# Kernel optimization log

Hardware: AMD Instinct MI355X
Metric: run time of the kernel (lower is better)

The kernel has to match this reference:

```python
import jax, jax.numpy as jnp
import numpy as np

N = 100000
H = 4      # heads
C = 32     # hidden per head (out_channels)
DIN = 9
NEG_SLOPE = 0.2  # PyG GATConv default


def gat_layer(x, src, dst, W, a_src, a_dst, b):
    # x: [N, F] -> h: [N, H, C]
    h = (x @ W).reshape(-1, H, C)
    s = (h * a_src).sum(-1)  # [N, H]
    d = (h * a_dst).sum(-1)  # [N, H]
    alpha = jax.nn.leaky_relu(s[src] + d[dst], negative_slope=NEG_SLOPE)  # [E, H]
    # segment softmax over incoming edges of each dst node
    amax = jax.ops.segment_max(alpha, dst, num_segments=N)
    e = jnp.exp(alpha - amax[dst])
    denom = jax.ops.segment_sum(e, dst, num_segments=N)
    w = e / denom[dst]                                   # [E, H]
    msg = h[src] * w[:, :, None]                          # [E, H, C]
    out = jax.ops.segment_sum(msg, dst, num_segments=N)  # [N, H, C]
    return out.mean(axis=1) + b                           # concat=False -> mean heads


def setup_inputs():
    key = jax.random.key(0)
    ks = jax.random.split(key, 16)
    E = 1600000
    EL = 500000
    sc = lambda *sh: 1.0 / np.sqrt(sh[0])
    inp = {
        "x": jax.random.normal(ks[0], (N, DIN), jnp.float32),
        "edge_index": jax.random.randint(ks[1], (2, E), 0, N, jnp.int32),
        "edge_label_index": jax.random.randint(ks[2], (2, EL), 0, N, jnp.int32),
        "W1": jax.random.normal(ks[3], (DIN, H * C), jnp.float32) * sc(DIN),
        "a_src1": jax.random.normal(ks[4], (H, C), jnp.float32) * sc(C),
        "a_dst1": jax.random.normal(ks[5], (H, C), jnp.float32) * sc(C),
        "b1": jnp.zeros((C,), jnp.float32),
        "W2": jax.random.normal(ks[6], (C, H * C), jnp.float32) * sc(C),
        "a_src2": jax.random.normal(ks[7], (H, C), jnp.float32) * sc(C),
        "a_dst2": jax.random.normal(ks[8], (H, C), jnp.float32) * sc(C),
        "b2": jnp.zeros((C,), jnp.float32),
        "Wn": jax.random.normal(ks[9], (C, 2), jnp.float32) * sc(C),
        "bn": jnp.zeros((2,), jnp.float32),
        "We1": jax.random.normal(ks[10], (2 * C, 64), jnp.float32) * sc(2 * C),
        "be1": jnp.zeros((64,), jnp.float32),
        "We2": jax.random.normal(ks[11], (64, 1), jnp.float32) * sc(64),
        "be2": jnp.zeros((1,), jnp.float32),
    }
    return inp


def reference(x, edge_index, edge_label_index, W1, a_src1, a_dst1, b1, W2, a_src2, a_dst2, b2, Wn, bn, We1, be1, We2, be2):
    # add self loops (PyG GATConv default)
    loop = jnp.arange(N, dtype=edge_index.dtype)
    src = jnp.concatenate([edge_index[0], loop])
    dst = jnp.concatenate([edge_index[1], loop])

    h = jax.nn.relu(gat_layer(x, src, dst, W1, a_src1, a_dst1, b1))
    h = jax.nn.relu(gat_layer(h, src, dst, W2, a_src2, a_dst2, b2))
    # dropout is identity in eval mode
    node_logits = h @ Wn + bn  # [N, 2]

    ei = jnp.concatenate([h[edge_label_index[0]], h[edge_label_index[1]]], axis=1)  # [EL, 2C]
    edge_logits = jax.nn.relu(ei @ We1 + be1) @ We2 + be2  # [EL, 1]
    return node_logits, edge_logits
```

## Files before the change

kernel.cpp:

```cpp
#include <hip/hip_runtime.h>
#include <hip/hip_fp16.h>


#define NPART 8
#define LOG2E 1.44269504088896f

using half8 = __attribute__((ext_vector_type(8))) _Float16;
using floatx4 = __attribute__((ext_vector_type(4))) float;

__global__ void init_pad_kernel(int* __restrict__ cnt, int* __restrict__ esrc_pad, int N) {
  int i = blockIdx.x * blockDim.x + threadIdx.x;
  if (i < N) {
    cnt[(size_t)i << 2] = 1;
    esrc_pad[(size_t)i << 6] = i;
  }
}

__global__ void scatter_pad_kernel(const int* __restrict__ src, const int* __restrict__ dst,
                                   int E, int* __restrict__ cnt, int* __restrict__ esrc_pad,
                                   int partSize) {
  int p = blockIdx.x & (NPART - 1);
  int sblk = blockIdx.x >> 3;
  int nsb = gridDim.x >> 3;
  int lo = p * partSize, hi = lo + partSize;
  int step = nsb * blockDim.x;
  int base = sblk * blockDim.x + threadIdx.x;
  int i = base;
  for (; i + 3 * step < E; i += 4 * step) {
    int i1 = i + step, i2 = i + 2 * step, i3 = i + 3 * step;
    int d0 = dst[i];
    int d1 = dst[i1];
    int d2 = dst[i2];
    int d3 = dst[i3];
    bool m0 = (d0 >= lo && d0 < hi);
    bool m1 = (d1 >= lo && d1 < hi);
    bool m2 = (d2 >= lo && d2 < hi);
    bool m3 = (d3 >= lo && d3 < hi);
    if (m0) {
      int pos = atomicAdd(&cnt[(size_t)d0 << 2], 1);
      if (pos < 64) esrc_pad[((size_t)d0 << 6) + pos] = src[i];
    }
    if (m1) {
      int pos = atomicAdd(&cnt[(size_t)d1 << 2], 1);
      if (pos < 64) esrc_pad[((size_t)d1 << 6) + pos] = src[i1];
    }
    if (m2) {
      int pos = atomicAdd(&cnt[(size_t)d2 << 2], 1);
      if (pos < 64) esrc_pad[((size_t)d2 << 6) + pos] = src[i2];
    }
    if (m3) {
      int pos = atomicAdd(&cnt[(size_t)d3 << 2], 1);
      if (pos < 64) esrc_pad[((size_t)d3 << 6) + pos] = src[i3];
    }
  }
  for (; i < E; i += step) {
    int dv = dst[i];
    if (dv >= lo && dv < hi) {
      int pos = atomicAdd(&cnt[(size_t)dv << 2], 1);
      if (pos < 64) esrc_pad[((size_t)dv << 6) + pos] = src[i];
    }
  }
}

template <bool L1>
__global__ __launch_bounds__(256) void transform_mfma_kernel(
    const float* __restrict__ xf, const __half* __restrict__ xh,
    const float* __restrict__ W, int Keff,
    const float* __restrict__ a_src, const float* __restrict__ a_dst,
    __half* __restrict__ h, float* __restrict__ s, float* __restrict__ d, int N) {
  int lane = threadIdx.x & 63;
  int quad = lane >> 4;
  int col = lane & 15;

  half8 af[8];
#pragma unroll
  for (int ct = 0; ct < 8; ++ct) {
#pragma unroll
    for (int j = 0; j < 8; ++j) {
      int k = quad * 8 + j;
      af[ct][j] = (k < Keff) ? (_Float16)W[k * 128 + ct * 16 + col] : (_Float16)0.f;
    }
  }

  int ntile = (N + 15) >> 4;
  int wstep = gridDim.x * 4;
  for (int tile = blockIdx.x * 4 + (threadIdx.x >> 6); tile < ntile; tile += wstep) {
    int node = tile * 16 + col;
    int nclamp = min(node, N - 1);

    half8 bfr;
    if (L1) {
      const float* xr = xf + (size_t)nclamp * 9;
#pragma unroll
      for (int j = 0; j < 8; ++j) {
        int k = quad * 8 + j;
        bfr[j] = (k < 9) ? (_Float16)xr[k] : (_Float16)0.f;
      }
    } else {
      bfr = *(const half8*)(xh + (size_t)nclamp * 32 + quad * 8);
    }

    floatx4 acc[8];
#pragma unroll
    for (int ct = 0; ct < 8; ++ct) acc[ct] = (floatx4){0.f, 0.f, 0.f, 0.f};
#pragma unroll
    for (int ct = 0; ct < 8; ++ct)
      acc[ct] = __builtin_amdgcn_mfma_f32_16x16x32_f16(af[ct], bfr, acc[ct], 0, 0, 0);

    float sp[4] = {0.f, 0.f, 0.f, 0.f}, dp[4] = {0.f, 0.f, 0.f, 0.f};
    bool wr = (node < N);
#pragma unroll
    for (int ct = 0; ct < 8; ++ct) {
      int f0 = ct * 16 + quad * 4;
      if (wr) {
        __half2 p0 = __floats2half2_rn(acc[ct][0], acc[ct][1]);
        __half2 p1 = __floats2half2_rn(acc[ct][2], acc[ct][3]);
        __half2* hp = (__half2*)(h + (size_t)node * 128 + f0);
        hp[0] = p0;
        hp[1] = p1;
      }
      int hh = ct >> 1;
      const float4 av = *(const float4*)(a_src + f0);
      const float4 dv = *(const float4*)(a_dst + f0);
      sp[hh] += acc[ct][0] * av.x + acc[ct][1] * av.y + acc[ct][2] * av.z + acc[ct][3] * av.w;
      dp[hh] += acc[ct][0] * dv.x + acc[ct][1] * dv.y + acc[ct][2] * dv.z + acc[ct][3] * dv.w;
    }
#pragma unroll
    for (int hh = 0; hh < 4; ++hh) {
      sp[hh] += __shfl_xor(sp[hh], 16);
      sp[hh] += __shfl_xor(sp[hh], 32);
      dp[hh] += __shfl_xor(dp[hh], 16);
      dp[hh] += __shfl_xor(dp[hh], 32);
    }
    if (quad == 0 && wr) {
      *(float4*)(s + node * 4) =
          make_float4(sp[0] * LOG2E, sp[1] * LOG2E, sp[2] * LOG2E, sp[3] * LOG2E);
      *(float4*)(d + node * 4) =
          make_float4(dp[0] * LOG2E, dp[1] * LOG2E, dp[2] * LOG2E, dp[3] * LOG2E);
    }
  }
}

__global__ void aggregate_kernel(const __half* __restrict__ h, const float* __restrict__ s,
                                 const float* __restrict__ d, const int* __restrict__ cntArr,
                                 const int* __restrict__ esrc, const float* __restrict__ bias,
                                 float* __restrict__ out, __half* __restrict__ out16,
                                 const float* __restrict__ Wn, const float* __restrict__ bn,
                                 float* __restrict__ out_node, int N) {
  int wid = blockIdx.x * (blockDim.x >> 6) + (threadIdx.x >> 6);
  if (wid >= N) return;
  int lane = threadIdx.x & 63;
  int g = lane >> 4;
  int k = lane & 15;
  int head = k >> 2;
  unsigned koff = (unsigned)k << 4;
  unsigned soff = (unsigned)head << 2;
  float dsel = d[wid * 4 + head];
  int beg = wid << 6;
  int cnt = min(cntArr[(size_t)wid << 2], 64);
  int end = beg + cnt;
  int M = (cnt + 3) >> 2;
  int i0 = beg + g;
  int last = end - 1;
  const char* hb = (const char*)h;
  const char* sb = (const char*)s;

  float acc[8] = {0.f, 0.f, 0.f, 0.f, 0.f, 0.f, 0.f, 0.f};
  float den = 0.f;

  int srcA = esrc[min(i0, last)];
  int srcB = esrc[min(i0 + 4, last)];
  float sv0 = *(const float*)(sb + (((unsigned)srcA << 4) + soff));
  half8 hv0 = *(const half8*)(hb + (((unsigned)srcA << 8) + koff));
  float sv1 = *(const float*)(sb + (((unsigned)srcB << 4) + soff));
  half8 hv1 = *(const half8*)(hb + (((unsigned)srcB << 8) + koff));
  srcA = esrc[min(i0 + 8, last)];
  srcB = esrc[min(i0 + 12, last)];

  int Mp = (M + 1) >> 1;
  for (int p = 0; p < Mp; ++p) {
    int t = 2 * p;
    {
      float a = sv0 + dsel;
      a = fmaxf(a, 0.2f * a);
      float e = __builtin_amdgcn_exp2f(a);
      e = (i0 + 4 * t < end) ? e : 0.f;
      den += e;
      const _Float16* hf = (const _Float16*)&hv0;
#pragma unroll
      for (int q = 0; q < 8; ++q)
        acc[q] = fmaf((float)hf[q], e, acc[q]);
    }
    sv0 = *(const float*)(sb + (((unsigned)srcA << 4) + soff));
    hv0 = *(const half8*)(hb + (((unsigned)srcA << 8) + koff));
    srcA = esrc[min(i0 + 4 * (t + 4), last)];
    {
      float a = sv1 + dsel;
      a = fmaxf(a, 0.2f * a);
      float e = __builtin_amdgcn_exp2f(a);
      e = (i0 + 4 * (t + 1) < end) ? e : 0.f;
      den += e;
      const _Float16* hf = (const _Float16*)&hv1;
#pragma unroll
      for (int q = 0; q < 8; ++q)
        acc[q] = fmaf((float)hf[q], e, acc[q]);
    }
    sv1 = *(const float*)(sb + (((unsigned)srcB << 4) + soff));
    hv1 = *(const half8*)(hb + (((unsigned)srcB << 8) + koff));
    srcB = esrc[min(i0 + 4 * (t + 5), last)];
  }

  den += __shfl_xor(den, 16);
  den += __shfl_xor(den, 32);
#pragma unroll
  for (int q = 0; q < 8; ++q) {
    acc[q] += __shfl_xor(acc[q], 16);
    acc[q] += __shfl_xor(acc[q], 32);
  }
  float inv = 1.f / den;
#pragma unroll
  for (int q = 0; q < 8; ++q) {
    acc[q] *= inv;
    acc[q] += __shfl_xor(acc[q], 4);
    acc[q] += __shfl_xor(acc[q], 8);
  }
  if (lane < 4) {
#pragma unroll
    for (int q = 0; q < 8; ++q)
      acc[q] = fmaxf(acc[q] * 0.25f + bias[8 * k + q], 0.f);
    if (out) {
      float4 o0 = make_float4(acc[0], acc[1], acc[2], acc[3]);
      float4 o1 = make_float4(acc[4], acc[5], acc[6], acc[7]);
      ((float4*)out)[(size_t)wid * 8 + 2 * k] = o0;
      ((float4*)out)[(size_t)wid * 8 + 2 * k + 1] = o1;
    }
    if (out16) {
      half8 hv;
#pragma unroll
      for (int q = 0; q < 8; ++q) hv[q] = (_Float16)acc[q];
      ((half8*)out16)[(size_t)wid * 4 + k] = hv;
    }
    if (Wn) {
      float p0 = 0.f, p1 = 0.f;
#pragma unroll
      for (int q = 0; q < 8; ++q) {
        int c = 8 * k + q;
        p0 = fmaf(acc[q], Wn[c * 2], p0);
        p1 = fmaf(acc[q], Wn[c * 2 + 1], p1);
      }
      p0 += __shfl_xor(p0, 1); p1 += __shfl_xor(p1, 1);
      p0 += __shfl_xor(p0, 2); p1 += __shfl_xor(p1, 2);
      if (k == 0) {
        out_node[wid * 2] = p0 + bn[0];
        out_node[wid * 2 + 1] = p1 + bn[1];
      }
    }
  }
}

__global__ __launch_bounds__(256) void edge_head_mfma_kernel(
    const __half* __restrict__ h2, const int* __restrict__ eli, int EL,
    const float* __restrict__ We1, const float* __restrict__ be1,
    const float* __restrict__ We2, const float* __restrict__ be2, float* __restrict__ out) {
  int lane = threadIdx.x & 63;
  int quad = lane >> 4;
  int col = lane & 15;

  half8 bf[2][4];
#pragma unroll
  for (int ks = 0; ks < 2; ++ks)
#pragma unroll
    for (int nt = 0; nt < 4; ++nt)
#pragma unroll
      for (int i = 0; i < 8; ++i)
        bf[ks][nt][i] = (_Float16)We1[(ks * 32 + quad * 8 + i) * 64 + nt * 16 + col];

  float b1v[4], w2v[4];
#pragma unroll
  for (int nt = 0; nt < 4; ++nt) {
    b1v[nt] = be1[nt * 16 + col];
    w2v[nt] = We2[nt * 16 + col];
  }
  float be2v = be2[0];

  int ngroups = (EL + 15) >> 4;
  int wstep = gridDim.x * 4;
  for (int group = blockIdx.x * 4 + (threadIdx.x >> 6); group < ngroups; group += wstep) {
    int e = min(group * 16 + col, EL - 1);
    int a = eli[e];
    int b = eli[EL + e];
    half8 af0 = *(const half8*)(h2 + (size_t)a * 32 + quad * 8);
    half8 af1 = *(const half8*)(h2 + (size_t)b * 32 + quad * 8);

    floatx4 acc[4];
#pragma unroll
    for (int nt = 0; nt < 4; ++nt) acc[nt] = (floatx4){0.f, 0.f, 0.f, 0.f};
#pragma unroll
    for (int nt = 0; nt < 4; ++nt)
      acc[nt] = __builtin_amdgcn_mfma_f32_16x16x32_f16(af0, bf[0][nt], acc[nt], 0, 0, 0);
#pragma unroll
    for (int nt = 0; nt < 4; ++nt)
      acc[nt] = __builtin_amdgcn_mfma_f32_16x16x32_f16(af1, bf[1][nt], acc[nt], 0, 0, 0);

#pragma unroll
    for (int reg = 0; reg < 4; ++reg) {
      float p = 0.f;
#pragma unroll
      for (int nt = 0; nt < 4; ++nt) {
        float z = acc[nt][reg] + b1v[nt];
        z = fmaxf(z, 0.f);
        p = fmaf(z, w2v[nt], p);
      }
      p += __shfl_xor(p, 1);
      p += __shfl_xor(p, 2);
      p += __shfl_xor(p, 4);
      p += __shfl_xor(p, 8);
      if (col == 0) {
        int eo = group * 16 + quad * 4 + reg;
        if (eo < EL) out[eo] = p + be2v;
      }
    }
  }
}

extern "C" void kernel_launch(void* const* d_in, const int* in_sizes, int n_in,
                              void* d_out, int out_size, void* d_ws, size_t ws_size,
                              hipStream_t stream) {
  const float* x = (const float*)d_in[0];
  const int* ei = (const int*)d_in[1];
  const int* eli = (const int*)d_in[2];
  const float* W1 = (const float*)d_in[3];
  const float* a_src1 = (const float*)d_in[4];
  const float* a_dst1 = (const float*)d_in[5];
  const float* b1 = (const float*)d_in[6];
  const float* W2 = (const float*)d_in[7];
  const float* a_src2 = (const float*)d_in[8];
  const float* a_dst2 = (const float*)d_in[9];
  const float* b2 = (const float*)d_in[10];
  const float* Wn = (const float*)d_in[11];
  const float* bn = (const float*)d_in[12];
  const float* We1 = (const float*)d_in[13];
  const float* be1 = (const float*)d_in[14];
  const float* We2 = (const float*)d_in[15];
  const float* be2 = (const float*)d_in[16];

  const int N = in_sizes[0] / 9;
  const int E = in_sizes[1] / 2;
  const int EL = in_sizes[2] / 2;

  float* wsf = (float*)d_ws;
  __half* h_half = (__half*)wsf;
  float* sbuf = wsf + (size_t)N * 64;
  float* dbuf = sbuf + (size_t)N * 4;
  __half* h1h = (__half*)(wsf + (size_t)N * 72);
  __half* h2h = h1h;
  int* cnt = (int*)(wsf + (size_t)N * 88);
  int* esrc_pad = cnt + (size_t)N * 4;

  float* out_node = (float*)d_out;
  float* out_edge = out_node + (size_t)N * 2;

  const int B = 256;
  const int wavesPerBlock = B / 64;
  int gridNwave = (N + wavesPerBlock - 1) / wavesPerBlock;
  int partSize = (N + NPART - 1) / NPART;
  int gridPart = NPART * 192;

  init_pad_kernel<<<(N + B - 1) / B, B, 0, stream>>>(cnt, esrc_pad, N);
  scatter_pad_kernel<<<gridPart, B, 0, stream>>>(ei, ei + E, E, cnt, esrc_pad, partSize);

  transform_mfma_kernel<true><<<512, B, 0, stream>>>(x, nullptr, W1, 9, a_src1, a_dst1,
                                                     h_half, sbuf, dbuf, N);
  aggregate_kernel<<<gridNwave, B, 0, stream>>>(h_half, sbuf, dbuf, cnt, esrc_pad, b1,
                                                nullptr, h1h, nullptr, nullptr, nullptr, N);

  transform_mfma_kernel<false><<<512, B, 0, stream>>>(nullptr, h1h, W2, 32, a_src2, a_dst2,
                                                      h_half, sbuf, dbuf, N);
  aggregate_kernel<<<gridNwave, B, 0, stream>>>(h_half, sbuf, dbuf, cnt, esrc_pad, b2,
                                                nullptr, h2h, Wn, bn, out_node, N);

  edge_head_mfma_kernel<<<1024, B, 0, stream>>>(h2h, eli, EL, We1, be1, We2, be2, out_edge);
}
```

Baseline: 378.6 us.

## Software-pipeline scatter atomics and deepen aggregate gather prefetch to four slots

The scatter kernel now double-buffers groups of four edges, so the atomics for the next group are issued before the esrc stores of the previous group, and it loads src together with dst. The aggregate kernel deepens its gather pipeline from two to four in-flight edges, clamps indices to the node range instead of the per-node edge range, and uses byte offsets with immediates. The workspace is reordered so cnt and esrc_pad come first, and the scatter grid grows from 1536 to 2048 blocks. The aim is to hide atomic and gather latency, at the cost of more registers and unconditional src loads for edges outside the partition.

Result: slower. 401.4 us (+6.0%).

```diff
diff --git a/kernel.cpp b/kernel.cpp
--- a/kernel.cpp
+++ b/kernel.cpp
@@ -25,41 +25,62 @@
   int lo = p * partSize, hi = lo + partSize;
   int step = nsb * blockDim.x;
   int base = sblk * blockDim.x + threadIdx.x;
-  int i = base;
-  for (; i + 3 * step < E; i += 4 * step) {
-    int i1 = i + step, i2 = i + 2 * step, i3 = i + 3 * step;
-    int d0 = dst[i];
-    int d1 = dst[i1];
-    int d2 = dst[i2];
-    int d3 = dst[i3];
-    bool m0 = (d0 >= lo && d0 < hi);
-    bool m1 = (d1 >= lo && d1 < hi);
-    bool m2 = (d2 >= lo && d2 < hi);
-    bool m3 = (d3 >= lo && d3 < hi);
-    if (m0) {
-      int pos = atomicAdd(&cnt[(size_t)d0 << 2], 1);
-      if (pos < 64) esrc_pad[((size_t)d0 << 6) + pos] = src[i];
-    }
-    if (m1) {
-      int pos = atomicAdd(&cnt[(size_t)d1 << 2], 1);
-      if (pos < 64) esrc_pad[((size_t)d1 << 6) + pos] = src[i1];
-    }
-    if (m2) {
-      int pos = atomicAdd(&cnt[(size_t)d2 << 2], 1);
-      if (pos < 64) esrc_pad[((size_t)d2 << 6) + pos] = src[i2];
-    }
-    if (m3) {
-      int pos = atomicAdd(&cnt[(size_t)d3 << 2], 1);
-      if (pos < 64) esrc_pad[((size_t)d3 << 6) + pos] = src[i3];
-    }
-  }
-  for (; i < E; i += step) {
-    int dv = dst[i];
-    if (dv >= lo && dv < hi) {
-      int pos = atomicAdd(&cnt[(size_t)dv << 2], 1);
-      if (pos < 64) esrc_pad[((size_t)dv << 6) + pos] = src[i];
-    }
-  }
+
+  int ad[4], asv[4], ap[4], am[4];
+  int bd[4], bsv[4], bp[4], bm[4];
+
+#pragma unroll
+  for (int u = 0; u < 4; ++u) {
+    int idx = base + u * step;
+    int ic = min(idx, E - 1);
+    ad[u] = dst[ic];
+    asv[u] = src[ic];
+    am[u] = (idx < E) & (ad[u] >= lo) & (ad[u] < hi);
+  }
+#pragma unroll
+  for (int u = 0; u < 4; ++u)
+    if (am[u]) ap[u] = atomicAdd(&cnt[(size_t)ad[u] << 2], 1);
+
+  int nitmax = (E + step - 1) / step;
+  int Gtot = (nitmax + 3) >> 2;
+  int P = Gtot >> 1;
+  int gb = base + 4 * step;
+
+  for (int pp = 0; pp < P; ++pp) {
+#pragma unroll
+    for (int u = 0; u < 4; ++u) {
+      int idx = gb + u * step;
+      int ic = min(idx, E - 1);
+      bd[u] = dst[ic];
+      bsv[u] = src[ic];
+      bm[u] = (idx < E) & (bd[u] >= lo) & (bd[u] < hi);
+    }
+#pragma unroll
+    for (int u = 0; u < 4; ++u)
+      if (bm[u]) bp[u] = atomicAdd(&cnt[(size_t)bd[u] << 2], 1);
+#pragma unroll
+    for (int u = 0; u < 4; ++u)
+      if (am[u] && ap[u] < 64) esrc_pad[((size_t)ad[u] << 6) + ap[u]] = asv[u];
+    gb += 4 * step;
+#pragma unroll
+    for (int u = 0; u < 4; ++u) {
+      int idx = gb + u * step;
+      int ic = min(idx, E - 1);
+      ad[u] = dst[ic];
+      asv[u] = src[ic];
+      am[u] = (idx < E) & (ad[u] >= lo) & (ad[u] < hi);
+    }
+#pragma unroll
+    for (int u = 0; u < 4; ++u)
+      if (am[u]) ap[u] = atomicAdd(&cnt[(size_t)ad[u] << 2], 1);
+#pragma unroll
+    for (int u = 0; u < 4; ++u)
+      if (bm[u] && bp[u] < 64) esrc_pad[((size_t)bd[u] << 6) + bp[u]] = bsv[u];
+    gb += 4 * step;
+  }
+#pragma unroll
+  for (int u = 0; u < 4; ++u)
+    if (am[u] && ap[u] < 64) esrc_pad[((size_t)ad[u] << 6) + ap[u]] = asv[u];
 }
 
 template <bool L1>
@@ -139,6 +160,11 @@
           make_float4(dp[0] * LOG2E, dp[1] * LOG2E, dp[2] * LOG2E, dp[3] * LOG2E);
     }
   }
+}
+
+__device__ __forceinline__ int ldclamp(const char* eb, unsigned off, int nlast) {
+  int v = *(const int*)(eb + off);
+  return min(max(v, 0), nlast);
 }
 
 __global__ void aggregate_kernel(const __half* __restrict__ h, const float* __restrict__ s,
@@ -156,59 +182,61 @@
   unsigned koff = (unsigned)k << 4;
   unsigned soff = (unsigned)head << 2;
   float dsel = d[wid * 4 + head];
-  int beg = wid << 6;
   int cnt = min(cntArr[(size_t)wid << 2], 64);
-  int end = beg + cnt;
   int M = (cnt + 3) >> 2;
-  int i0 = beg + g;
-  int last = end - 1;
+  int Mq = (M + 3) >> 2;
+  int nlast = N - 1;
   const char* hb = (const char*)h;
   const char* sb = (const char*)s;
+  const char* eb = (const char*)esrc;
+  unsigned eoff = ((unsigned)(wid * 64 + g)) << 2;
 
   float acc[8] = {0.f, 0.f, 0.f, 0.f, 0.f, 0.f, 0.f, 0.f};
   float den = 0.f;
 
-  int srcA = esrc[min(i0, last)];
-  int srcB = esrc[min(i0 + 4, last)];
-  float sv0 = *(const float*)(sb + (((unsigned)srcA << 4) + soff));
-  half8 hv0 = *(const half8*)(hb + (((unsigned)srcA << 8) + koff));
-  float sv1 = *(const float*)(sb + (((unsigned)srcB << 4) + soff));
-  half8 hv1 = *(const half8*)(hb + (((unsigned)srcB << 8) + koff));
-  srcA = esrc[min(i0 + 8, last)];
-  srcB = esrc[min(i0 + 12, last)];
-
-  int Mp = (M + 1) >> 1;
-  for (int p = 0; p < Mp; ++p) {
-    int t = 2 * p;
-    {
-      float a = sv0 + dsel;
-      a = fmaxf(a, 0.2f * a);
-      float e = __builtin_amdgcn_exp2f(a);
-      e = (i0 + 4 * t < end) ? e : 0.f;
-      den += e;
-      const _Float16* hf = (const _Float16*)&hv0;
-#pragma unroll
-      for (int q = 0; q < 8; ++q)
-        acc[q] = fmaf((float)hf[q], e, acc[q]);
-    }
-    sv0 = *(const float*)(sb + (((unsigned)srcA << 4) + soff));
-    hv0 = *(const half8*)(hb + (((unsigned)srcA << 8) + koff));
-    srcA = esrc[min(i0 + 4 * (t + 4), last)];
-    {
-      float a = sv1 + dsel;
-      a = fmaxf(a, 0.2f * a);
-      float e = __builtin_amdgcn_exp2f(a);
-      e = (i0 + 4 * (t + 1) < end) ? e : 0.f;
-      den += e;
-      const _Float16* hf = (const _Float16*)&hv1;
-#pragma unroll
-      for (int q = 0; q < 8; ++q)
-        acc[q] = fmaf((float)hf[q], e, acc[q]);
-    }
-    sv1 = *(const float*)(sb + (((unsigned)srcB << 4) + soff));
-    hv1 = *(const half8*)(hb + (((unsigned)srcB << 8) + koff));
-    srcB = esrc[min(i0 + 4 * (t + 5), last)];
-  }
+  int s0 = ldclamp(eb, eoff + 0, nlast);
+  int s1 = ldclamp(eb, eoff + 16, nlast);
+  int s2 = ldclamp(eb, eoff + 32, nlast);
+  int s3 = ldclamp(eb, eoff + 48, nlast);
+  float sv0 = *(const float*)(sb + ((unsigned)s0 << 4) + soff);
+  half8 hv0 = *(const half8*)(hb + ((unsigned)s0 << 8) + koff);
+  float sv1 = *(const float*)(sb + ((unsigned)s1 << 4) + soff);
+  half8 hv1 = *(const half8*)(hb + ((unsigned)s1 << 8) + koff);
+  float sv2 = *(const float*)(sb + ((unsigned)s2 << 4) + soff);
+  half8 hv2 = *(const half8*)(hb + ((unsigned)s2 << 8) + koff);
+  float sv3 = *(const float*)(sb + ((unsigned)s3 << 4) + soff);
+  half8 hv3 = *(const half8*)(hb + ((unsigned)s3 << 8) + koff);
+  s0 = ldclamp(eb, eoff + 64, nlast);
+  s1 = ldclamp(eb, eoff + 80, nlast);
+  s2 = ldclamp(eb, eoff + 96, nlast);
+  s3 = ldclamp(eb, eoff + 112, nlast);
+
+  int lim = cnt - g;
+
+#define AGG_STEP(SV, HV, SRC, JLIT, IMM)                                        \
+  {                                                                             \
+    float a = (SV) + dsel;                                                      \
+    a = fmaxf(a, 0.2f * a);                                                     \
+    float e = __builtin_amdgcn_exp2f(a);                                        \
+    e = ((JLIT) < lim) ? e : 0.f;                                               \
+    den += e;                                                                   \
+    const _Float16* hf = (const _Float16*)&(HV);                                \
+    _Pragma("unroll") for (int q = 0; q < 8; ++q)                               \
+        acc[q] = fmaf((float)hf[q], e, acc[q]);           \
+  }                                                                             \
+  (SV) = *(const float*)(sb + ((unsigned)(SRC) << 4) + soff);                   \
+  (HV) = *(const half8*)(hb + ((unsigned)(SRC) << 8) + koff);                   \
+  (SRC) = ldclamp(eb, eoff + (IMM), nlast);
+
+  for (int p = 0; p < Mq; ++p) {
+    AGG_STEP(sv0, hv0, s0, 0, 128)
+    AGG_STEP(sv1, hv1, s1, 4, 144)
+    AGG_STEP(sv2, hv2, s2, 8, 160)
+    AGG_STEP(sv3, hv3, s3, 12, 176)
+    eoff += 64;
+    lim -= 16;
+  }
+#undef AGG_STEP
 
   den += __shfl_xor(den, 16);
   den += __shfl_xor(den, 32);
@@ -349,13 +377,13 @@
   const int EL = in_sizes[2] / 2;
 
   float* wsf = (float*)d_ws;
-  __half* h_half = (__half*)wsf;
-  float* sbuf = wsf + (size_t)N * 64;
+  int* cnt = (int*)wsf;
+  int* esrc_pad = cnt + (size_t)N * 4;
+  __half* h_half = (__half*)(wsf + (size_t)N * 68);
+  float* sbuf = wsf + (size_t)N * 132;
   float* dbuf = sbuf + (size_t)N * 4;
-  __half* h1h = (__half*)(wsf + (size_t)N * 72);
+  __half* h1h = (__half*)(wsf + (size_t)N * 140);
   __half* h2h = h1h;
-  int* cnt = (int*)(wsf + (size_t)N * 88);
-  int* esrc_pad = cnt + (size_t)N * 4;
 
   float* out_node = (float*)d_out;
   float* out_edge = out_node + (size_t)N * 2;
@@ -364,7 +392,7 @@
   const int wavesPerBlock = B / 64;
   int gridNwave = (N + wavesPerBlock - 1) / wavesPerBlock;
   int partSize = (N + NPART - 1) / NPART;
-  int gridPart = NPART * 192;
+  int gridPart = NPART * 256;
 
   init_pad_kernel<<<(N + B - 1) / B, B, 0, stream>>>(cnt, esrc_pad, N);
   scatter_pad_kernel<<<gridPart, B, 0, stream>>>(ei, ei + E, E, cnt, esrc_pad, partSize);
```
